# Kernel optimization log

Hardware: AMD Instinct MI355X
Metric: run time of the kernel (lower is better)

The kernel has to match this reference:

```python
import jax, jax.numpy as jnp
import numpy as np


def setup_inputs() -> dict:
    key = jax.random.key(0)
    ks = jax.random.split(key, 7)
    B, S, D, KP = 16, 4096, 64, 256  # batch*heads, seq_len, head_dim, linformer proj dim
    Q = jax.random.normal(ks[0], (B, S, D), dtype=jnp.float32)
    K = jax.random.normal(ks[1], (B, S, D), dtype=jnp.float32)
    V = jax.random.normal(ks[2], (B, S, D), dtype=jnp.float32)
    E_w = jax.random.normal(ks[3], (KP, S), dtype=jnp.float32) / np.sqrt(S)
    E_b = jax.random.normal(ks[4], (KP,), dtype=jnp.float32) * 0.01
    F_w = jax.random.normal(ks[5], (KP, S), dtype=jnp.float32) / np.sqrt(S)
    F_b = jax.random.normal(ks[6], (KP,), dtype=jnp.float32) * 0.01
    return {"Q": Q, "K": K, "V": V, "E_w": E_w, "E_b": E_b, "F_w": F_w, "F_b": F_b}


def reference(Q, K, V, E_w, E_b, F_w, F_b):
    # Linformer head (mask=None path); dropout is identity at inference.
    dim_k = K.shape[-1]
    scale = 1.0 / jnp.sqrt(jnp.float32(dim_k))
    # K.permute(0,2,1) -> [B, d, S]; E projects seq axis S -> k: [B, d, k]
    Kp = jnp.einsum('bsd,ks->bdk', K, E_w) + E_b  # [B, d, k]
    # V.permute -> F -> permute back: [B, k, d]
    Vp = jnp.einsum('bsd,ks->bkd', V, F_w) + F_b[None, :, None]  # [B, k, d]
    scores = jnp.einsum('bsd,bdk->bsk', Q, Kp) * scale  # [B, S, k]
    attn = jax.nn.softmax(scores, axis=-1)
    out = jnp.einsum('bsk,bkd->bsd', attn, Vp)  # [B, S, d]
    return (out, attn)
```

## Files before the change

kernel.cpp:

```cpp
#include <hip/hip_runtime.h>


#define B_  16
#define S_  4096
#define D_  64
#define KP_ 256

typedef short v8s __attribute__((ext_vector_type(8)));
typedef float v4f __attribute__((ext_vector_type(4)));

__device__ __forceinline__ short f2bf(float x) {
    union { float f; unsigned u; } v; v.f = x;
    unsigned r = v.u + 0x7FFFu + ((v.u >> 16) & 1u);
    return (short)(r >> 16);
}
__device__ __forceinline__ float bf2f(short h) {
    union { float f; unsigned u; } v; v.u = ((unsigned)(unsigned short)h) << 16;
    return v.f;
}

__global__ __launch_bounds__(256)
void wcvt_kernel(const float* __restrict__ E_w, const float* __restrict__ F_w,
                 short* __restrict__ Whi, short* __restrict__ Wlo)
{
    const int p = blockIdx.y;
    const float* W = p ? F_w : E_w;
    const size_t i4 = (size_t)blockIdx.x * 256 + threadIdx.x;
    float4 v = ((const float4*)W)[i4];
    short4 h, lo;
    h.x = f2bf(v.x); lo.x = f2bf(v.x - bf2f(h.x));
    h.y = f2bf(v.y); lo.y = f2bf(v.y - bf2f(h.y));
    h.z = f2bf(v.z); lo.z = f2bf(v.z - bf2f(h.z));
    h.w = f2bf(v.w); lo.w = f2bf(v.w - bf2f(h.w));
    const size_t o = (size_t)p * (KP_ * S_) + i4 * 4;
    *(short4*)(Whi + o) = h;
    *(short4*)(Wlo + o) = lo;
}

__global__ __launch_bounds__(512, 2)
void proj_mfma_kernel(const float* __restrict__ Kg, const float* __restrict__ Vg,
                      const short* __restrict__ Whi, const short* __restrict__ Wlo,
                      float* __restrict__ PpartK, float* __restrict__ PpartV)
{
    const int sc = blockIdx.x;
    const int p  = blockIdx.y;
    const int b  = blockIdx.z;

    const float* src = (p ? Vg : Kg) + ((size_t)b * S_ + sc * 512) * D_;
    const short* Wh = Whi + (size_t)p * KP_ * S_ + sc * 512;
    const short* Wl = Wlo + (size_t)p * KP_ * S_ + sc * 512;

    __shared__ __align__(16) short Af[2][2][4][512];

    const int t  = threadIdx.x;
    const int wv = t >> 6;
    const int l  = t & 63;

    v4f acc[2][4];
#pragma unroll
    for (int i = 0; i < 2; ++i)
#pragma unroll
        for (int m = 0; m < 4; ++m) acc[i][m] = (v4f){0.f, 0.f, 0.f, 0.f};

    const bool do_stage = (t < 256);
    const int sd   = t & 63;
    const int soct = (t >> 6) & 3;
    const int smt  = sd >> 4;
    const int sfl  = (sd & 15) + soct * 16;

    float g[8];
    if (do_stage) {
        const float* sp = src + (size_t)(soct * 8) * D_ + sd;
#pragma unroll
        for (int j = 0; j < 8; ++j) g[j] = sp[(size_t)j * D_];
        v8s hi, lo;
#pragma unroll
        for (int j = 0; j < 8; ++j) { short h = f2bf(g[j]); hi[j] = h; lo[j] = f2bf(g[j] - bf2f(h)); }
        *(v8s*)&Af[0][0][smt][sfl * 8] = hi;
        *(v8s*)&Af[0][1][smt][sfl * 8] = lo;
    }
    __syncthreads();

    const int krow0 = wv * 32;

    for (int st = 0; st < 16; ++st) {
        const int cur = st & 1;
        if (st + 1 < 16 && do_stage) {
            const float* sp = src + (size_t)((st + 1) * 32 + soct * 8) * D_ + sd;
#pragma unroll
            for (int j = 0; j < 8; ++j) g[j] = sp[(size_t)j * D_];
        }
        v8s wh[2], wl2[2];
#pragma unroll
        for (int i = 0; i < 2; ++i) {
            size_t off = (size_t)(krow0 + i * 16 + (l & 15)) * S_ + st * 32 + (l >> 4) * 8;
            wh[i]  = *(const v8s*)(Wh + off);
            wl2[i] = *(const v8s*)(Wl + off);
        }
        v8s sh[4], sl[4];
#pragma unroll
        for (int m = 0; m < 4; ++m) {
            sh[m] = *(const v8s*)&Af[cur][0][m][l * 8];
            sl[m] = *(const v8s*)&Af[cur][1][m][l * 8];
        }
        if (p == 0) {
#pragma unroll
            for (int i = 0; i < 2; ++i)
#pragma unroll
                for (int m = 0; m < 4; ++m) {
                    acc[i][m] = __builtin_amdgcn_mfma_f32_16x16x32_bf16(wh[i],  sh[m], acc[i][m], 0, 0, 0);
                    acc[i][m] = __builtin_amdgcn_mfma_f32_16x16x32_bf16(wh[i],  sl[m], acc[i][m], 0, 0, 0);
                    acc[i][m] = __builtin_amdgcn_mfma_f32_16x16x32_bf16(wl2[i], sh[m], acc[i][m], 0, 0, 0);
                }
        } else {
#pragma unroll
            for (int i = 0; i < 2; ++i)
#pragma unroll
                for (int m = 0; m < 4; ++m) {
                    acc[i][m] = __builtin_amdgcn_mfma_f32_16x16x32_bf16(sh[m], wh[i],  acc[i][m], 0, 0, 0);
                    acc[i][m] = __builtin_amdgcn_mfma_f32_16x16x32_bf16(sl[m], wh[i],  acc[i][m], 0, 0, 0);
                    acc[i][m] = __builtin_amdgcn_mfma_f32_16x16x32_bf16(sh[m], wl2[i], acc[i][m], 0, 0, 0);
                }
        }
        if (st + 1 < 16 && do_stage) {
            v8s hi, lo;
#pragma unroll
            for (int j = 0; j < 8; ++j) { short h = f2bf(g[j]); hi[j] = h; lo[j] = f2bf(g[j] - bf2f(h)); }
            *(v8s*)&Af[cur ^ 1][0][smt][sfl * 8] = hi;
            *(v8s*)&Af[cur ^ 1][1][smt][sfl * 8] = lo;
        }
        __syncthreads();
    }

    if (p == 0) {
        float* outp = PpartK + ((size_t)sc * B_ + b) * (KP_ * D_);
#pragma unroll
        for (int i = 0; i < 2; ++i)
#pragma unroll
            for (int m = 0; m < 4; ++m)
#pragma unroll
                for (int r = 0; r < 4; ++r) {
                    int k = krow0 + i * 16 + (l >> 4) * 4 + r;
                    int d = m * 16 + (l & 15);
                    outp[(size_t)k * D_ + d] = acc[i][m][r];
                }
    } else {
        float* outp = PpartV + ((size_t)sc * B_ + b) * (KP_ * D_);
#pragma unroll
        for (int i = 0; i < 2; ++i)
#pragma unroll
            for (int m = 0; m < 4; ++m)
#pragma unroll
                for (int r = 0; r < 4; ++r) {
                    int d = m * 16 + (l >> 4) * 4 + r;
                    int k = krow0 + i * 16 + (l & 15);
                    outp[(size_t)d * KP_ + k] = acc[i][m][r];
                }
    }
}

__global__ __launch_bounds__(256)
void reduce_kernel(const float* __restrict__ PpartK, const float* __restrict__ PpartV,
                   const float* __restrict__ E_b, const float* __restrict__ F_b,
                   short* __restrict__ Kp_hi, short* __restrict__ Kp_lo,
                   short* __restrict__ Vp_hi)
{
    const int j    = blockIdx.x * 256 + threadIdx.x;
    const int side = j >> 16;
    const int i4   = j & 65535;
    const int flat = i4 * 4;
    const int b    = flat >> 14;
    const int dk   = flat & 16383;

    if (side == 0) {
        float4 a = make_float4(0.f, 0.f, 0.f, 0.f);
#pragma unroll
        for (int sc = 0; sc < 8; ++sc) {
            float4 v = *(const float4*)(PpartK + ((size_t)sc * B_ + b) * (KP_ * D_) + dk);
            a.x += v.x; a.y += v.y; a.z += v.z; a.w += v.w;
        }
        float be = E_b[dk >> 6];
        a.x += be; a.y += be; a.z += be; a.w += be;
        short4 h, lo;
        h.x = f2bf(a.x); lo.x = f2bf(a.x - bf2f(h.x));
        h.y = f2bf(a.y); lo.y = f2bf(a.y - bf2f(h.y));
        h.z = f2bf(a.z); lo.z = f2bf(a.z - bf2f(h.z));
        h.w = f2bf(a.w); lo.w = f2bf(a.w - bf2f(h.w));
        *(short4*)(Kp_hi + (size_t)b * 16384 + dk) = h;
        *(short4*)(Kp_lo + (size_t)b * 16384 + dk) = lo;
    } else {
        float4 a = make_float4(0.f, 0.f, 0.f, 0.f);
#pragma unroll
        for (int sc = 0; sc < 8; ++sc) {
            float4 v = *(const float4*)(PpartV + ((size_t)sc * B_ + b) * (KP_ * D_) + dk);
            a.x += v.x; a.y += v.y; a.z += v.z; a.w += v.w;
        }
        float4 bf = *(const float4*)(F_b + (dk & 255));
        a.x += bf.x; a.y += bf.y; a.z += bf.z; a.w += bf.w;
        short4 h;
        h.x = f2bf(a.x); h.y = f2bf(a.y); h.z = f2bf(a.z); h.w = f2bf(a.w);
        *(short4*)(Vp_hi + (size_t)b * 16384 + dk) = h;
    }
}

__global__ __launch_bounds__(256, 4)
void attn_mfma_kernel(const float* __restrict__ Qg,
                      const short* __restrict__ Kp_hi, const short* __restrict__ Kp_lo,
                      const short* __restrict__ Vp_hi,
                      float* __restrict__ attn_out, float* __restrict__ outg)
{
    const int st = blockIdx.x;
    const int b  = blockIdx.y;
    const int t  = threadIdx.x;
    const int wv = t >> 6;
    const int l  = t & 63;

    __shared__ __align__(16) short smem[64 * 264];
    short (*Qf)[2][4][512] = (short (*)[2][4][512])smem;
    short* Pl = smem;

    {
        const int s    = t & 63;
        const int doct = t >> 6;
        const float* qrow = Qg + ((size_t)b * S_ + st * 64 + s) * D_;
        const int mt = s >> 4, fl = (s & 15) + doct * 16;
#pragma unroll
        for (int kd = 0; kd < 2; ++kd) {
            float4 v0 = *(const float4*)(qrow + kd * 32 + doct * 8);
            float4 v1 = *(const float4*)(qrow + kd * 32 + doct * 8 + 4);
            float gq[8] = {v0.x, v0.y, v0.z, v0.w, v1.x, v1.y, v1.z, v1.w};
            v8s hi, lo;
#pragma unroll
            for (int jj = 0; jj < 8; ++jj) { short h = f2bf(gq[jj]); hi[jj] = h; lo[jj] = f2bf(gq[jj] - bf2f(h)); }
            *(v8s*)&Qf[kd][0][mt][fl * 8] = hi;
            *(v8s*)&Qf[kd][1][mt][fl * 8] = lo;
        }
    }
    __syncthreads();

    v4f acc2[16];
#pragma unroll
    for (int nt = 0; nt < 16; ++nt) acc2[nt] = (v4f){0.f, 0.f, 0.f, 0.f};
    const size_t kb = (size_t)b * (KP_ * D_);
#pragma unroll
    for (int kd = 0; kd < 2; ++kd) {
        v8s Ah = *(const v8s*)&Qf[kd][0][wv][l * 8];
        v8s Al = *(const v8s*)&Qf[kd][1][wv][l * 8];
#pragma unroll
        for (int nt = 0; nt < 16; ++nt) {
            size_t off = kb + (size_t)(nt * 16 + (l & 15)) * D_ + kd * 32 + (l >> 4) * 8;
            v8s Bh = *(const v8s*)(Kp_hi + off);
            v8s Bl = *(const v8s*)(Kp_lo + off);
            acc2[nt] = __builtin_amdgcn_mfma_f32_16x16x32_bf16(Ah, Bh, acc2[nt], 0, 0, 0);
            acc2[nt] = __builtin_amdgcn_mfma_f32_16x16x32_bf16(Al, Bh, acc2[nt], 0, 0, 0);
            acc2[nt] = __builtin_amdgcn_mfma_f32_16x16x32_bf16(Ah, Bl, acc2[nt], 0, 0, 0);
        }
    }
    __syncthreads();

    const float scale = 0.125f;
    float* attn_b = attn_out + ((size_t)b * S_ + st * 64) * KP_;
#pragma unroll
    for (int r = 0; r < 4; ++r) {
        float m = -3.4e38f;
#pragma unroll
        for (int nt = 0; nt < 16; ++nt) m = fmaxf(m, acc2[nt][r]);
        m = fmaxf(m, __shfl_xor(m, 1));
        m = fmaxf(m, __shfl_xor(m, 2));
        m = fmaxf(m, __shfl_xor(m, 4));
        m = fmaxf(m, __shfl_xor(m, 8));
        float sum = 0.f;
#pragma unroll
        for (int nt = 0; nt < 16; ++nt) {
            float e = __expf((acc2[nt][r] - m) * scale);
            acc2[nt][r] = e; sum += e;
        }
        sum += __shfl_xor(sum, 1);
        sum += __shfl_xor(sum, 2);
        sum += __shfl_xor(sum, 4);
        sum += __shfl_xor(sum, 8);
        const float inv = 1.f / sum;
        const int s_loc = wv * 16 + (l >> 4) * 4 + r;
#pragma unroll
        for (int nt = 0; nt < 16; ++nt) {
            float pv = acc2[nt][r] * inv;
            attn_b[(size_t)s_loc * KP_ + nt * 16 + (l & 15)] = pv;
            Pl[s_loc * 264 + nt * 16 + (l & 15)] = f2bf(pv);
        }
    }
    v4f acc3[4];
#pragma unroll
    for (int nt = 0; nt < 4; ++nt) acc3[nt] = (v4f){0.f, 0.f, 0.f, 0.f};
#pragma unroll
    for (int kc = 0; kc < 8; ++kc) {
        v8s A3 = *(const v8s*)&Pl[(wv * 16 + (l & 15)) * 264 + kc * 32 + (l >> 4) * 8];
#pragma unroll
        for (int nt = 0; nt < 4; ++nt) {
            size_t off = kb + (size_t)(nt * 16 + (l & 15)) * KP_ + kc * 32 + (l >> 4) * 8;
            v8s B3 = *(const v8s*)(Vp_hi + off);
            acc3[nt] = __builtin_amdgcn_mfma_f32_16x16x32_bf16(A3, B3, acc3[nt], 0, 0, 0);
        }
    }
    float* out_b = outg + ((size_t)b * S_ + st * 64) * D_;
#pragma unroll
    for (int nt = 0; nt < 4; ++nt)
#pragma unroll
        for (int r = 0; r < 4; ++r) {
            int s_loc = wv * 16 + (l >> 4) * 4 + r;
            out_b[(size_t)s_loc * D_ + nt * 16 + (l & 15)] = acc3[nt][r];
        }
}

extern "C" void kernel_launch(void* const* d_in, const int* in_sizes, int n_in,
                              void* d_out, int out_size, void* d_ws, size_t ws_size,
                              hipStream_t stream) {
    const float* Q   = (const float*)d_in[0];
    const float* K   = (const float*)d_in[1];
    const float* V   = (const float*)d_in[2];
    const float* E_w = (const float*)d_in[3];
    const float* E_b = (const float*)d_in[4];
    const float* F_w = (const float*)d_in[5];
    const float* F_b = (const float*)d_in[6];

    float* out  = (float*)d_out;
    float* attn = out + (size_t)B_ * S_ * D_;

    short* Whi   = (short*)d_ws;
    short* Wlo   = Whi + (size_t)2 * KP_ * S_;
    short* Kp_hi = Wlo + (size_t)2 * KP_ * S_;
    short* Kp_lo = Kp_hi + (size_t)B_ * KP_ * D_;
    short* Vp_hi = Kp_lo + (size_t)B_ * KP_ * D_;

    float* PpartK = attn;
    float* PpartV = attn + (size_t)8 * B_ * KP_ * D_;

    wcvt_kernel<<<dim3(KP_ * S_ / 4 / 256, 2), 256, 0, stream>>>(E_w, F_w, Whi, Wlo);
    proj_mfma_kernel<<<dim3(8, 2, B_), 512, 0, stream>>>(K, V, Whi, Wlo, PpartK, PpartV);
    reduce_kernel<<<dim3(512), 256, 0, stream>>>(PpartK, PpartV, E_b, F_b, Kp_hi, Kp_lo, Vp_hi);
    attn_mfma_kernel<<<dim3(S_ / 64, B_), 256, 0, stream>>>(Q, Kp_hi, Kp_lo, Vp_hi, attn, out);
}
```

Measured before the change: 216.7 us.

## Pre-swizzle Kp/Vp into MFMA fragment layout and stage attn stores through LDS

The finalize kernel now writes Kp and Vp in per-fragment 512-element tiles, so each lane in the attention kernel loads its MFMA B operand with one contiguous 16-byte access instead of strided rows. The attention output is staged through a per-wave LDS buffer and written back as row-contiguous float4 stores, replacing scattered scalar stores. The extra LDS lowers the occupancy hint from 4 to 3 blocks per CU, and the in-wave LDS staging depends on wave-synchronous execution with no barrier.

```diff
diff --git a/kernel.cpp b/kernel.cpp
--- a/kernel.cpp
+++ b/kernel.cpp
@@ -179,15 +179,18 @@
             float4 v = *(const float4*)(PpartK + ((size_t)sc * B_ + b) * (KP_ * D_) + dk);
             a.x += v.x; a.y += v.y; a.z += v.z; a.w += v.w;
         }
-        float be = E_b[dk >> 6];
+        const int k = dk >> 6, d = dk & 63;
+        float be = E_b[k];
         a.x += be; a.y += be; a.z += be; a.w += be;
         short4 h, lo;
         h.x = f2bf(a.x); lo.x = f2bf(a.x - bf2f(h.x));
         h.y = f2bf(a.y); lo.y = f2bf(a.y - bf2f(h.y));
         h.z = f2bf(a.z); lo.z = f2bf(a.z - bf2f(h.z));
         h.w = f2bf(a.w); lo.w = f2bf(a.w - bf2f(h.w));
-        *(short4*)(Kp_hi + (size_t)b * 16384 + dk) = h;
-        *(short4*)(Kp_lo + (size_t)b * 16384 + dk) = lo;
+        const size_t fo = (((size_t)b * 2 + (d >> 5)) * 16 + (k >> 4)) * 512
+                        + (size_t)((k & 15) + ((d >> 3) & 3) * 16) * 8 + (d & 7);
+        *(short4*)(Kp_hi + fo) = h;
+        *(short4*)(Kp_lo + fo) = lo;
     } else {
         float4 a = make_float4(0.f, 0.f, 0.f, 0.f);
 #pragma unroll
@@ -195,15 +198,18 @@
             float4 v = *(const float4*)(PpartV + ((size_t)sc * B_ + b) * (KP_ * D_) + dk);
             a.x += v.x; a.y += v.y; a.z += v.z; a.w += v.w;
         }
-        float4 bf = *(const float4*)(F_b + (dk & 255));
+        const int d = dk >> 8, k = dk & 255;
+        float4 bf = *(const float4*)(F_b + k);
         a.x += bf.x; a.y += bf.y; a.z += bf.z; a.w += bf.w;
         short4 h;
         h.x = f2bf(a.x); h.y = f2bf(a.y); h.z = f2bf(a.z); h.w = f2bf(a.w);
-        *(short4*)(Vp_hi + (size_t)b * 16384 + dk) = h;
-    }
-}
-
-__global__ __launch_bounds__(256, 4)
+        const size_t fo = (((size_t)b * 8 + (k >> 5)) * 4 + (d >> 4)) * 512
+                        + (size_t)((d & 15) + ((k >> 3) & 3) * 16) * 8 + (k & 7);
+        *(short4*)(Vp_hi + fo) = h;
+    }
+}
+
+__global__ __launch_bounds__(256, 3)
 void attn_mfma_kernel(const float* __restrict__ Qg,
                       const short* __restrict__ Kp_hi, const short* __restrict__ Kp_lo,
                       const short* __restrict__ Vp_hi,
@@ -216,6 +222,7 @@
     const int l  = t & 63;
 
     __shared__ __align__(16) short smem[64 * 264];
+    __shared__ __align__(16) float Fst[4][4][264];
     short (*Qf)[2][4][512] = (short (*)[2][4][512])smem;
     short* Pl = smem;
 
@@ -241,14 +248,13 @@
     v4f acc2[16];
 #pragma unroll
     for (int nt = 0; nt < 16; ++nt) acc2[nt] = (v4f){0.f, 0.f, 0.f, 0.f};
-    const size_t kb = (size_t)b * (KP_ * D_);
 #pragma unroll
     for (int kd = 0; kd < 2; ++kd) {
         v8s Ah = *(const v8s*)&Qf[kd][0][wv][l * 8];
         v8s Al = *(const v8s*)&Qf[kd][1][wv][l * 8];
 #pragma unroll
         for (int nt = 0; nt < 16; ++nt) {
-            size_t off = kb + (size_t)(nt * 16 + (l & 15)) * D_ + kd * 32 + (l >> 4) * 8;
+            size_t off = (((size_t)b * 2 + kd) * 16 + nt) * 512 + (size_t)l * 8;
             v8s Bh = *(const v8s*)(Kp_hi + off);
             v8s Bl = *(const v8s*)(Kp_lo + off);
             acc2[nt] = __builtin_amdgcn_mfma_f32_16x16x32_bf16(Ah, Bh, acc2[nt], 0, 0, 0);
@@ -260,6 +266,7 @@
 
     const float scale = 0.125f;
     float* attn_b = attn_out + ((size_t)b * S_ + st * 64) * KP_;
+    const int g = l >> 4;
 #pragma unroll
     for (int r = 0; r < 4; ++r) {
         float m = -3.4e38f;
@@ -280,12 +287,17 @@
         sum += __shfl_xor(sum, 4);
         sum += __shfl_xor(sum, 8);
         const float inv = 1.f / sum;
-        const int s_loc = wv * 16 + (l >> 4) * 4 + r;
+        const int s_loc = wv * 16 + g * 4 + r;
 #pragma unroll
         for (int nt = 0; nt < 16; ++nt) {
             float pv = acc2[nt][r] * inv;
-            attn_b[(size_t)s_loc * KP_ + nt * 16 + (l & 15)] = pv;
+            Fst[wv][g][nt * 16 + (l & 15)] = pv;
             Pl[s_loc * 264 + nt * 16 + (l & 15)] = f2bf(pv);
+        }
+#pragma unroll
+        for (int gg = 0; gg < 4; ++gg) {
+            float4 vv = *(const float4*)&Fst[wv][gg][l * 4];
+            *(float4*)(attn_b + (size_t)(wv * 16 + gg * 4 + r) * KP_ + l * 4) = vv;
         }
     }
     v4f acc3[4];
@@ -296,7 +308,7 @@
         v8s A3 = *(const v8s*)&Pl[(wv * 16 + (l & 15)) * 264 + kc * 32 + (l >> 4) * 8];
 #pragma unroll
         for (int nt = 0; nt < 4; ++nt) {
-            size_t off = kb + (size_t)(nt * 16 + (l & 15)) * KP_ + kc * 32 + (l >> 4) * 8;
+            size_t off = (((size_t)b * 8 + kc) * 4 + nt) * 512 + (size_t)l * 8;
             v8s B3 = *(const v8s*)(Vp_hi + off);
             acc3[nt] = __builtin_amdgcn_mfma_f32_16x16x32_bf16(A3, B3, acc3[nt], 0, 0, 0);
         }
```

Result: faster. 200.1 us (-7.7%).
